# Kernel tuning notes

Hardware: AMD Instinct MI355X
Metric: run time of the kernel (lower is better)

The kernel has to match this reference:

```python
import jax, jax.numpy as jnp
import numpy as np

N_NODES = 50000
N_EDGES = 800000
IN_DIM, HID_DIM, OUT_DIM = 128, 128, 256


def _gcn_conv(x, W, b, src, dst, num_nodes):
    # PyG GCNConv: h = D^{-1/2} (A + I) D^{-1/2} X W + b (self-loops already in src/dst)
    h = x @ W  # (N, F_out)
    ones = jnp.ones(src.shape[0], dtype=h.dtype)
    deg = jax.ops.segment_sum(ones, dst, num_segments=num_nodes)
    dinv = jnp.where(deg > 0, jax.lax.rsqrt(deg), 0.0)
    norm = dinv[src] * dinv[dst]  # (E,)
    msg = h[src] * norm[:, None]  # (E, F_out) gather
    out = jax.ops.segment_sum(msg, dst, num_segments=num_nodes)  # scatter-add
    return out + b


def setup_inputs() -> dict:
    key = jax.random.key(0)
    ks = jax.random.split(key, 6)
    x = jax.random.normal(ks[0], (N_NODES, IN_DIM), dtype=jnp.float32)
    edge_index = jax.random.randint(ks[1], (2, N_EDGES), 0, N_NODES, dtype=jnp.int64)
    W1 = jax.random.normal(ks[2], (IN_DIM, HID_DIM), dtype=jnp.float32) / np.sqrt(IN_DIM)
    b1 = jnp.zeros((HID_DIM,), jnp.float32)
    W2 = jax.random.normal(ks[3], (HID_DIM, OUT_DIM), dtype=jnp.float32) / np.sqrt(HID_DIM)
    b2 = jnp.zeros((OUT_DIM,), jnp.float32)
    Wa = jax.random.normal(ks[4], (OUT_DIM, 1), dtype=jnp.float32) / np.sqrt(OUT_DIM)
    ba = jnp.zeros((1,), jnp.float32)
    return {"x": x, "edge_index": edge_index, "W1": W1, "b1": b1, "W2": W2, "b2": b2, "Wa": Wa, "ba": ba}


def reference(x, edge_index, W1, b1, W2, b2, Wa, ba):
    n = x.shape[0]
    loops = jnp.arange(n, dtype=edge_index.dtype)
    src = jnp.concatenate([edge_index[0], loops])
    dst = jnp.concatenate([edge_index[1], loops])
    h = jax.nn.relu(_gcn_conv(x, W1, b1, src, dst, n))
    # dropout is a no-op in eval mode
    node_embeddings = jax.nn.relu(_gcn_conv(h, W2, b2, src, dst, n))
    logits = node_embeddings @ Wa + ba  # (N, 1)
    attn = jax.nn.softmax(logits, axis=0)  # softmax over nodes
    graph_embedding = jnp.sum(node_embeddings * attn, axis=0, keepdims=True)  # (1, OUT_DIM)
    return (node_embeddings, graph_embedding)
```

## Files before the change

### kernel.cpp

```cpp
#include <hip/hip_runtime.h>
#include <hip/hip_fp16.h>
#include <math.h>

typedef __attribute__((ext_vector_type(8))) short bf16x8;
typedef __attribute__((ext_vector_type(4))) float f32x4;

static __device__ __forceinline__ unsigned short f2bf(float x) {
    unsigned u = __float_as_uint(x);
    unsigned r = (u + 0x7FFF + ((u >> 16) & 1)) >> 16;
    return (unsigned short)r;
}
static __device__ __forceinline__ float bf2f(unsigned short h) {
    return __uint_as_float(((unsigned)h) << 16);
}
static __device__ __forceinline__ void addh8(float* a, uint4 v) {
    float2 f;
    f = __half22float2(*(const __half2*)&v.x); a[0] += f.x; a[1] += f.y;
    f = __half22float2(*(const __half2*)&v.y); a[2] += f.x; a[3] += f.y;
    f = __half22float2(*(const __half2*)&v.z); a[4] += f.x; a[5] += f.y;
    f = __half22float2(*(const __half2*)&v.w); a[6] += f.x; a[7] += f.y;
}


__global__ __launch_bounds__(256) void count_deg_kernel(const int* __restrict__ dst, int E,
                                                        int* __restrict__ deg,
                                                        int* __restrict__ epos) {
    int e = blockIdx.x * 256 + threadIdx.x;
    if (e < E) epos[e] = atomicAdd(&deg[dst[e]], 1);
}

__global__ __launch_bounds__(256) void scan_partial_kernel(const int* __restrict__ deg, int n,
                                                           int* __restrict__ partials) {
    int idx = blockIdx.x * 1024 + threadIdx.x * 4;
    int4 v = make_int4(0, 0, 0, 0);
    if (idx + 3 < n) v = *(const int4*)(deg + idx);
    else {
        if (idx < n) v.x = deg[idx];
        if (idx + 1 < n) v.y = deg[idx + 1];
        if (idx + 2 < n) v.z = deg[idx + 2];
    }
    int s = v.x + v.y + v.z + v.w;
    for (int off = 1; off < 64; off <<= 1) s += __shfl_xor(s, off);
    __shared__ int sm[4];
    int wave = threadIdx.x >> 6;
    if ((threadIdx.x & 63) == 0) sm[wave] = s;
    __syncthreads();
    if (threadIdx.x == 0) partials[blockIdx.x] = sm[0] + sm[1] + sm[2] + sm[3];
}

__global__ __launch_bounds__(256) void scan_final_kernel(const int* __restrict__ deg, int n,
                                                         const int* __restrict__ partials, int nbk,
                                                         int* __restrict__ rowptr) {
    int idx = blockIdx.x * 1024 + threadIdx.x * 4;
    int4 v = make_int4(0, 0, 0, 0);
    if (idx + 3 < n) v = *(const int4*)(deg + idx);
    else {
        if (idx < n) v.x = deg[idx];
        if (idx + 1 < n) v.y = deg[idx + 1];
        if (idx + 2 < n) v.z = deg[idx + 2];
    }
    int tsum = v.x + v.y + v.z + v.w;
    int lane = threadIdx.x & 63, wave = threadIdx.x >> 6;
    int s = tsum;
    for (int off = 1; off < 64; off <<= 1) {
        int u = __shfl_up(s, off);
        if (lane >= off) s += u;
    }
    __shared__ int wsum[4];
    __shared__ int bb;
    if (lane == 63) wsum[wave] = s;
    if (threadIdx.x < 64) {
        int pv = (threadIdx.x < nbk) ? partials[threadIdx.x] : 0;
        int ps = pv;
        for (int off = 1; off < 64; off <<= 1) {
            int u = __shfl_up(ps, off);
            if (threadIdx.x >= off) ps += u;
        }
        if (threadIdx.x == blockIdx.x) bb = ps - pv;
        if (blockIdx.x == 0 && threadIdx.x == 63) rowptr[n] = ps;
    }
    __syncthreads();
    int base = bb;
    for (int w = 0; w < wave; ++w) base += wsum[w];
    int e0 = base + s - tsum;
    int4 o;
    o.x = e0; o.y = e0 + v.x; o.z = o.y + v.y; o.w = o.z + v.z;
    if (idx + 3 < n) *(int4*)(rowptr + idx) = o;
    else {
        if (idx < n) rowptr[idx] = o.x;
        if (idx + 1 < n) rowptr[idx + 1] = o.y;
        if (idx + 2 < n) rowptr[idx + 2] = o.z;
    }
}


__global__ __launch_bounds__(256) void prep_kernel(
    const int* __restrict__ src, const int* __restrict__ dst, const int* __restrict__ epos, int E,
    const int* __restrict__ rowptr, int* __restrict__ csrsrc, int scatterBlocks,
    const float* __restrict__ x, float* __restrict__ dinv,
    __half2* __restrict__ xs16, int n, int prescaleBlocks,
    const float* __restrict__ W1, const float* __restrict__ W2,
    unsigned short* __restrict__ w1h, unsigned short* __restrict__ w1l,
    unsigned short* __restrict__ w2h, unsigned short* __restrict__ w2l) {
    int b = blockIdx.x;
    if (b < scatterBlocks) {
        int e = b * 256 + threadIdx.x;
        if (e < E) csrsrc[rowptr[dst[e]] + epos[e]] = src[e];
    } else if (b < scatterBlocks + prescaleBlocks) {
        int node = (b - scatterBlocks) * 4 + (threadIdx.x >> 6);
        int lane = threadIdx.x & 63;
        if (node >= n) return;
        float di = rsqrtf((float)(rowptr[node + 1] - rowptr[node] + 1));
        if (lane == 0) dinv[node] = di;
        float2 v = *(const float2*)(x + (size_t)node * 128 + (lane << 1));
        xs16[(size_t)node * 64 + lane] = __floats2half2_rn(di * v.x, di * v.y);
    } else {
        int i = (b - scatterBlocks - prescaleBlocks) * 256 + threadIdx.x;
        if (i < 128 * 128) {
            int nn = i >> 7, k = i & 127;
            float v = W1[k * 128 + nn];
            unsigned short h = f2bf(v);
            w1h[nn * 128 + k] = h;
            w1l[nn * 128 + k] = f2bf(v - bf2f(h));
        } else if (i < 128 * 128 + 256 * 128) {
            int j = i - 128 * 128;
            int nn = j >> 7, k = j & 127;
            float v = W2[k * 256 + nn];
            unsigned short h = f2bf(v);
            w2h[nn * 128 + k] = h;
            w2l[nn * 128 + k] = f2bf(v - bf2f(h));
        }
    }
}


template <int NCOLS, bool SCALE_DINV, bool DO_LOGITS, bool OUT_F16>
__global__ __launch_bounds__(512, 2) void fused_gemm(
    const unsigned short* __restrict__ X16,
    const int* __restrict__ rowptr, const int* __restrict__ csrsrc,
    const float* __restrict__ dinv,
    const unsigned short* __restrict__ Bth, const unsigned short* __restrict__ Btl,
    const float* __restrict__ bias, void* __restrict__ Cout, int M,
    const float* __restrict__ Wa, float* __restrict__ logits) {
    constexpr int CT = NCOLS / 64;
    __shared__ unsigned short AsH[128 * 128];
    __shared__ unsigned short AsL[128 * 128];

    const int t = threadIdx.x;
    const int row0 = blockIdx.x * 128;

    {
        const int nl = t >> 2;
        const int sub = t & 3;
        const int row = row0 + nl;
        float acc[32];
#pragma unroll
        for (int i = 0; i < 32; ++i) acc[i] = 0.f;
        float di = 0.f;
        if (row < M) {
            const uint4* __restrict__ Xv = (const uint4*)X16;
            size_t sb = (size_t)row * 16 + sub * 4;
            uint4 v0 = Xv[sb], v1 = Xv[sb + 1], v2 = Xv[sb + 2], v3 = Xv[sb + 3];
            addh8(acc, v0); addh8(acc + 8, v1); addh8(acc + 16, v2); addh8(acc + 24, v3);
            int e1 = rowptr[row + 1];
            int e = rowptr[row];
            for (; e + 2 <= e1; e += 2) {
                int s0 = csrsrc[e], s1 = csrsrc[e + 1];
                size_t b0 = (size_t)s0 * 16 + sub * 4;
                size_t b1 = (size_t)s1 * 16 + sub * 4;
                uint4 a0 = Xv[b0], a1 = Xv[b0 + 1], a2 = Xv[b0 + 2], a3 = Xv[b0 + 3];
                uint4 c0 = Xv[b1], c1 = Xv[b1 + 1], c2 = Xv[b1 + 2], c3 = Xv[b1 + 3];
                addh8(acc, a0); addh8(acc + 8, a1); addh8(acc + 16, a2); addh8(acc + 24, a3);
                addh8(acc, c0); addh8(acc + 8, c1); addh8(acc + 16, c2); addh8(acc + 24, c3);
            }
            if (e < e1) {
                size_t b0 = (size_t)csrsrc[e] * 16 + sub * 4;
                uint4 a0 = Xv[b0], a1 = Xv[b0 + 1], a2 = Xv[b0 + 2], a3 = Xv[b0 + 3];
                addh8(acc, a0); addh8(acc + 8, a1); addh8(acc + 16, a2); addh8(acc + 24, a3);
            }
            di = dinv[row];
        }
#pragma unroll
        for (int j = 0; j < 4; ++j) {
            int ga = sub * 4 + j;
            int off = nl * 128 + (ga >> 3) * 64 + (((ga & 7) ^ (nl & 7)) << 3);
            unsigned short h[8], l[8];
#pragma unroll
            for (int q = 0; q < 8; ++q) {
                float f = di * acc[j * 8 + q];
                h[q] = f2bf(f);
                l[q] = f2bf(f - bf2f(h[q]));
            }
            uint4 hv, lv;
            hv.x = (unsigned)h[0] | ((unsigned)h[1] << 16);
            hv.y = (unsigned)h[2] | ((unsigned)h[3] << 16);
            hv.z = (unsigned)h[4] | ((unsigned)h[5] << 16);
            hv.w = (unsigned)h[6] | ((unsigned)h[7] << 16);
            lv.x = (unsigned)l[0] | ((unsigned)l[1] << 16);
            lv.y = (unsigned)l[2] | ((unsigned)l[3] << 16);
            lv.z = (unsigned)l[4] | ((unsigned)l[5] << 16);
            lv.w = (unsigned)l[6] | ((unsigned)l[7] << 16);
            *(uint4*)(AsH + off) = hv;
            *(uint4*)(AsL + off) = lv;
        }
    }
    __syncthreads();

    const int lane = t & 63;
    const int wave = t >> 6;
    const int wrow = wave >> 2;
    const int wcol = wave & 3;
    const int lq = lane >> 4;
    const int lm = lane & 15;

    f32x4 acc2[4][CT] = {};
    float lacc[4][4] = {};

#pragma unroll
    for (int kc = 0; kc < 2; ++kc)
#pragma unroll
        for (int ks = 0; ks < 2; ++ks) {
            const int gbase = ks * 4 + lq;
            bf16x8 ah[4], al[4], bh[CT], bl[CT];
#pragma unroll
            for (int rt = 0; rt < 4; ++rt) {
                int ra = wrow * 64 + rt * 16 + lm;
                int off = ra * 128 + kc * 64 + ((gbase ^ (ra & 7)) << 3);
                ah[rt] = *(const bf16x8*)(AsH + off);
                al[rt] = *(const bf16x8*)(AsL + off);
            }
#pragma unroll
            for (int ct = 0; ct < CT; ++ct) {
                int col = wcol * (16 * CT) + ct * 16 + lm;
                size_t bo = (size_t)col * 128 + kc * 64 + gbase * 8;
                bh[ct] = *(const bf16x8*)(Bth + bo);
                bl[ct] = *(const bf16x8*)(Btl + bo);
            }
#pragma unroll
            for (int rt = 0; rt < 4; ++rt)
#pragma unroll
                for (int ct = 0; ct < CT; ++ct) {
                    acc2[rt][ct] = __builtin_amdgcn_mfma_f32_16x16x32_bf16(ah[rt], bh[ct], acc2[rt][ct], 0, 0, 0);
                    acc2[rt][ct] = __builtin_amdgcn_mfma_f32_16x16x32_bf16(al[rt], bh[ct], acc2[rt][ct], 0, 0, 0);
                    acc2[rt][ct] = __builtin_amdgcn_mfma_f32_16x16x32_bf16(ah[rt], bl[ct], acc2[rt][ct], 0, 0, 0);
                }
        }

#pragma unroll
    for (int ct = 0; ct < CT; ++ct) {
        int col = wcol * (16 * CT) + ct * 16 + lm;
        float bc = bias[col];
        float wac = DO_LOGITS ? Wa[col] : 0.f;
#pragma unroll
        for (int rt = 0; rt < 4; ++rt) {
            int rowb = row0 + wrow * 64 + rt * 16 + lq * 4;
#pragma unroll
            for (int reg = 0; reg < 4; ++reg) {
                int gr = rowb + reg;
                if (gr < M) {
                    float o = fmaxf(acc2[rt][ct][reg] + bc, 0.f);
                    if (SCALE_DINV) o *= dinv[gr];
                    if (OUT_F16) ((__half*)Cout)[(size_t)gr * NCOLS + col] = __float2half(o);
                    else ((float*)Cout)[(size_t)gr * NCOLS + col] = o;
                    if (DO_LOGITS) lacc[rt][reg] += o * wac;
                }
            }
        }
    }

    if (DO_LOGITS) {
#pragma unroll
        for (int rt = 0; rt < 4; ++rt)
#pragma unroll
            for (int reg = 0; reg < 4; ++reg) {
                float s = lacc[rt][reg];
                s += __shfl_xor(s, 1);
                s += __shfl_xor(s, 2);
                s += __shfl_xor(s, 4);
                s += __shfl_xor(s, 8);
                int gr = row0 + wrow * 64 + rt * 16 + lq * 4 + reg;
                if (lm == 0 && gr < M) atomicAdd(&logits[gr], s);
            }
    }
}


__global__ __launch_bounds__(256) void maxsum_kernel(const float* __restrict__ logits, int n,
                                                     float2* __restrict__ part,
                                                     float* __restrict__ outTail) {
    if (blockIdx.x == 0) outTail[threadIdx.x] = 0.f;
    float m = -INFINITY, s = 0.f;
    for (int i = blockIdx.x * 256 + threadIdx.x; i < n; i += gridDim.x * 256) {
        float v = logits[i];
        if (v > m) { s = s * expf(m - v) + 1.f; m = v; }
        else s += expf(v - m);
    }
    __shared__ float sm[256], ss[256];
    sm[threadIdx.x] = m; ss[threadIdx.x] = s;
    __syncthreads();
    for (int off = 128; off > 0; off >>= 1) {
        if (threadIdx.x < off) {
            float m1 = sm[threadIdx.x], s1 = ss[threadIdx.x];
            float m2 = sm[threadIdx.x + off], s2 = ss[threadIdx.x + off];
            float M = fmaxf(m1, m2);
            sm[threadIdx.x] = M;
            ss[threadIdx.x] = s1 * expf(m1 - M) + s2 * expf(m2 - M);
        }
        __syncthreads();
    }
    if (threadIdx.x == 0) part[blockIdx.x] = make_float2(sm[0], ss[0]);
}

static __device__ __forceinline__ float2 merge_part(const float2* __restrict__ part, int t,
                                                    float* red2) {
    if (t < 64) {
        float2 p = part[t];
        float m = p.x, s = p.y;
        for (int off = 32; off > 0; off >>= 1) {
            float m2 = __shfl_xor(m, off);
            float s2 = __shfl_xor(s, off);
            float M = fmaxf(m, m2);
            s = s * expf(m - M) + s2 * expf(m2 - M);
            m = M;
        }
        if (t == 0) { red2[0] = m; red2[1] = s; }
    }
    __syncthreads();
    return make_float2(red2[0], red2[1]);
}

__global__ __launch_bounds__(256) void weighted_sum_kernel(const float* __restrict__ emb,
                                                           const float* __restrict__ logits,
                                                           const float2* __restrict__ part,
                                                           float* __restrict__ gpart, int n) {
    __shared__ float red2[2];
    float g = merge_part(part, threadIdx.x, red2).x;
    int wave = threadIdx.x >> 6;
    int lane = threadIdx.x & 63;
    int stride = gridDim.x * 4;
    float4 acc = make_float4(0.f, 0.f, 0.f, 0.f);
#pragma unroll 2
    for (int r = blockIdx.x * 4 + wave; r < n; r += stride) {
        float w = expf(logits[r] - g);
        float4 v = *(const float4*)(emb + (size_t)r * 256 + (lane << 2));
        acc.x += w * v.x; acc.y += w * v.y; acc.z += w * v.z; acc.w += w * v.w;
    }
    __shared__ float4 sm[256];
    sm[threadIdx.x] = acc;
    __syncthreads();
    if (wave == 0) {
        float4 a = sm[lane], b = sm[64 + lane], c = sm[128 + lane], d = sm[192 + lane];
        float4 s;
        s.x = (a.x + b.x) + (c.x + d.x);
        s.y = (a.y + b.y) + (c.y + d.y);
        s.z = (a.z + b.z) + (c.z + d.z);
        s.w = (a.w + b.w) + (c.w + d.w);
        *(float4*)(gpart + (size_t)blockIdx.x * 256 + (lane << 2)) = s;
    }
}

__global__ __launch_bounds__(256) void reduce_gpart_kernel(const float* __restrict__ gpart,
                                                           const float2* __restrict__ part,
                                                           float* __restrict__ outTail, int nb) {
    __shared__ float red2[2];
    float gsum = merge_part(part, threadIdx.x, red2).y;
    int rows = nb / gridDim.x;
    int r0 = blockIdx.x * rows;
    float s = 0.f;
    for (int r = r0; r < r0 + rows; ++r) s += gpart[(size_t)r * 256 + threadIdx.x];
    atomicAdd(&outTail[threadIdx.x], s / gsum);
}


extern "C" void kernel_launch(void* const* d_in, const int* in_sizes, int n_in,
                              void* d_out, int out_size, void* d_ws, size_t ws_size,
                              hipStream_t stream) {
    const float* x  = (const float*)d_in[0];
    const int* ei   = (const int*)d_in[1];
    const float* W1 = (const float*)d_in[2];
    const float* b1 = (const float*)d_in[3];
    const float* W2 = (const float*)d_in[4];
    const float* b2 = (const float*)d_in[5];
    const float* Wa = (const float*)d_in[6];
    float* out = (float*)d_out;

    const int n = in_sizes[0] / 128;
    const int E = in_sizes[1] / 2;
    const int* srcA = ei;
    const int* dstA = ei + E;
    const int nb = (n + 1023) / 1024;
    const int WS_BLOCKS = 1024;

    unsigned short* xs16 = (unsigned short*)d_ws;
    unsigned short* h16  = xs16 + (size_t)n * 128;
    unsigned short* w1h  = h16 + (size_t)n * 128;
    unsigned short* w1l  = w1h + 128 * 128;
    unsigned short* w2h  = w1l + 128 * 128;
    unsigned short* w2l  = w2h + 256 * 128;
    float* dinv   = (float*)(w2l + 256 * 128);
    float* logits = dinv + n;
    int* deg      = (int*)(logits + n);
    int* rowptr   = deg + n;
    int* partials = rowptr + n + 1;
    float2* part  = (float2*)(partials + 64);
    float* gpart  = (float*)(part + 64);
    int* epos     = (int*)(gpart + WS_BLOCKS * 256);
    int* csrsrc   = epos + E;

    hipMemsetAsync(logits, 0, sizeof(float) * (size_t)(2 * n), stream);

    count_deg_kernel<<<(E + 255) / 256, 256, 0, stream>>>(dstA, E, deg, epos);
    scan_partial_kernel<<<nb, 256, 0, stream>>>(deg, n, partials);
    scan_final_kernel<<<nb, 256, 0, stream>>>(deg, n, partials, nb, rowptr);

    int scatterBlocks = (E + 255) / 256;
    int prescaleBlocks = (n + 3) / 4;
    int wconvBlocks = (128 * 128 + 256 * 128 + 255) / 256;
    prep_kernel<<<scatterBlocks + prescaleBlocks + wconvBlocks, 256, 0, stream>>>(
        srcA, dstA, epos, E, rowptr, csrsrc, scatterBlocks,
        x, dinv, (__half2*)xs16, n, prescaleBlocks,
        W1, W2, w1h, w1l, w2h, w2l);

    int gemmRows = (n + 127) / 128;

    fused_gemm<128, true, false, true><<<gemmRows, 512, 0, stream>>>(
        xs16, rowptr, csrsrc, dinv, w1h, w1l, b1, h16, n, nullptr, nullptr);
    fused_gemm<256, false, true, false><<<gemmRows, 512, 0, stream>>>(
        h16, rowptr, csrsrc, dinv, w2h, w2l, b2, out, n, Wa, logits);

    maxsum_kernel<<<64, 256, 0, stream>>>(logits, n, part, out + (size_t)n * 256);
    weighted_sum_kernel<<<WS_BLOCKS, 256, 0, stream>>>(out, logits, part, gpart, n);
    reduce_gpart_kernel<<<32, 256, 0, stream>>>(gpart, part, out + (size_t)n * 256, WS_BLOCKS);
}
```

Measured before the change: 296.8 us.

## Halve fused GEMM row tile to 64 and raise occupancy with 8 threads per node

The fused aggregate+GEMM kernel now processes 64 rows per block instead of 128, with 8 threads per node each gathering 16 features and the edge loop unrolled by 4. The wave layout changes so each wave owns one 16-row strip and half the output columns, which shrinks the accumulator register footprint and LDS use. Launch bounds go from 2 to 8 blocks per CU to raise occupancy and hide gather latency. The cost is less reuse of B fragments per wave, more B loads from global/L2 per MFMA, and more blocks overall.

```diff
diff --git a/kernel.cpp b/kernel.cpp
--- a/kernel.cpp
+++ b/kernel.cpp
@@ -135,54 +135,60 @@
 
 
 template <int NCOLS, bool SCALE_DINV, bool DO_LOGITS, bool OUT_F16>
-__global__ __launch_bounds__(512, 2) void fused_gemm(
+__global__ __launch_bounds__(512, 8) void fused_gemm(
     const unsigned short* __restrict__ X16,
     const int* __restrict__ rowptr, const int* __restrict__ csrsrc,
     const float* __restrict__ dinv,
     const unsigned short* __restrict__ Bth, const unsigned short* __restrict__ Btl,
     const float* __restrict__ bias, void* __restrict__ Cout, int M,
     const float* __restrict__ Wa, float* __restrict__ logits) {
-    constexpr int CT = NCOLS / 64;
-    __shared__ unsigned short AsH[128 * 128];
-    __shared__ unsigned short AsL[128 * 128];
+    constexpr int CT = NCOLS / 32;
+    __shared__ unsigned short AsH[64 * 128];
+    __shared__ unsigned short AsL[64 * 128];
 
     const int t = threadIdx.x;
-    const int row0 = blockIdx.x * 128;
+    const int row0 = blockIdx.x * 64;
 
     {
-        const int nl = t >> 2;
-        const int sub = t & 3;
+        const int nl = t >> 3;
+        const int sub = t & 7;
         const int row = row0 + nl;
-        float acc[32];
-#pragma unroll
-        for (int i = 0; i < 32; ++i) acc[i] = 0.f;
+        float acc[16];
+#pragma unroll
+        for (int i = 0; i < 16; ++i) acc[i] = 0.f;
         float di = 0.f;
         if (row < M) {
             const uint4* __restrict__ Xv = (const uint4*)X16;
-            size_t sb = (size_t)row * 16 + sub * 4;
-            uint4 v0 = Xv[sb], v1 = Xv[sb + 1], v2 = Xv[sb + 2], v3 = Xv[sb + 3];
-            addh8(acc, v0); addh8(acc + 8, v1); addh8(acc + 16, v2); addh8(acc + 24, v3);
+            size_t sb = (size_t)row * 16 + sub * 2;
+            uint4 v0 = Xv[sb], v1 = Xv[sb + 1];
+            addh8(acc, v0); addh8(acc + 8, v1);
             int e1 = rowptr[row + 1];
             int e = rowptr[row];
-            for (; e + 2 <= e1; e += 2) {
-                int s0 = csrsrc[e], s1 = csrsrc[e + 1];
-                size_t b0 = (size_t)s0 * 16 + sub * 4;
-                size_t b1 = (size_t)s1 * 16 + sub * 4;
-                uint4 a0 = Xv[b0], a1 = Xv[b0 + 1], a2 = Xv[b0 + 2], a3 = Xv[b0 + 3];
-                uint4 c0 = Xv[b1], c1 = Xv[b1 + 1], c2 = Xv[b1 + 2], c3 = Xv[b1 + 3];
-                addh8(acc, a0); addh8(acc + 8, a1); addh8(acc + 16, a2); addh8(acc + 24, a3);
-                addh8(acc, c0); addh8(acc + 8, c1); addh8(acc + 16, c2); addh8(acc + 24, c3);
+            for (; e + 4 <= e1; e += 4) {
+                int s0 = csrsrc[e], s1 = csrsrc[e + 1], s2 = csrsrc[e + 2], s3 = csrsrc[e + 3];
+                size_t b0 = (size_t)s0 * 16 + sub * 2;
+                size_t b1 = (size_t)s1 * 16 + sub * 2;
+                size_t b2 = (size_t)s2 * 16 + sub * 2;
+                size_t b3 = (size_t)s3 * 16 + sub * 2;
+                uint4 a0 = Xv[b0], a1 = Xv[b0 + 1];
+                uint4 c0 = Xv[b1], c1 = Xv[b1 + 1];
+                uint4 d0 = Xv[b2], d1 = Xv[b2 + 1];
+                uint4 f0 = Xv[b3], f1 = Xv[b3 + 1];
+                addh8(acc, a0); addh8(acc + 8, a1);
+                addh8(acc, c0); addh8(acc + 8, c1);
+                addh8(acc, d0); addh8(acc + 8, d1);
+                addh8(acc, f0); addh8(acc + 8, f1);
             }
-            if (e < e1) {
-                size_t b0 = (size_t)csrsrc[e] * 16 + sub * 4;
-                uint4 a0 = Xv[b0], a1 = Xv[b0 + 1], a2 = Xv[b0 + 2], a3 = Xv[b0 + 3];
-                addh8(acc, a0); addh8(acc + 8, a1); addh8(acc + 16, a2); addh8(acc + 24, a3);
+            for (; e < e1; ++e) {
+                size_t b0 = (size_t)csrsrc[e] * 16 + sub * 2;
+                uint4 a0 = Xv[b0], a1 = Xv[b0 + 1];
+                addh8(acc, a0); addh8(acc + 8, a1);
             }
             di = dinv[row];
         }
 #pragma unroll
-        for (int j = 0; j < 4; ++j) {
-            int ga = sub * 4 + j;
+        for (int j = 0; j < 2; ++j) {
+            int ga = sub * 2 + j;
             int off = nl * 128 + (ga >> 3) * 64 + (((ga & 7) ^ (nl & 7)) << 3);
             unsigned short h[8], l[8];
 #pragma unroll
@@ -208,79 +214,65 @@
 
     const int lane = t & 63;
     const int wave = t >> 6;
-    const int wrow = wave >> 2;
-    const int wcol = wave & 3;
+    const int wrow = wave & 3;
+    const int wcol = wave >> 2;
     const int lq = lane >> 4;
     const int lm = lane & 15;
 
-    f32x4 acc2[4][CT] = {};
-    float lacc[4][4] = {};
+    f32x4 acc2[CT] = {};
+    float lacc[4] = {0.f, 0.f, 0.f, 0.f};
 
 #pragma unroll
     for (int kc = 0; kc < 2; ++kc)
 #pragma unroll
         for (int ks = 0; ks < 2; ++ks) {
             const int gbase = ks * 4 + lq;
-            bf16x8 ah[4], al[4], bh[CT], bl[CT];
-#pragma unroll
-            for (int rt = 0; rt < 4; ++rt) {
-                int ra = wrow * 64 + rt * 16 + lm;
-                int off = ra * 128 + kc * 64 + ((gbase ^ (ra & 7)) << 3);
-                ah[rt] = *(const bf16x8*)(AsH + off);
-                al[rt] = *(const bf16x8*)(AsL + off);
+            const int ra = wrow * 16 + lm;
+            const int aoff = ra * 128 + kc * 64 + ((gbase ^ (ra & 7)) << 3);
+            bf16x8 ah = *(const bf16x8*)(AsH + aoff);
+            bf16x8 al = *(const bf16x8*)(AsL + aoff);
+#pragma unroll
+            for (int ct = 0; ct < CT; ++ct) {
+                int col = wcol * (NCOLS / 2) + ct * 16 + lm;
+                size_t bo = (size_t)col * 128 + kc * 64 + gbase * 8;
+                bf16x8 bh = *(const bf16x8*)(Bth + bo);
+                bf16x8 bl = *(const bf16x8*)(Btl + bo);
+                acc2[ct] = __builtin_amdgcn_mfma_f32_16x16x32_bf16(ah, bh, acc2[ct], 0, 0, 0);
+                acc2[ct] = __builtin_amdgcn_mfma_f32_16x16x32_bf16(al, bh, acc2[ct], 0, 0, 0);
+                acc2[ct] = __builtin_amdgcn_mfma_f32_16x16x32_bf16(ah, bl, acc2[ct], 0, 0, 0);
             }
-#pragma unroll
-            for (int ct = 0; ct < CT; ++ct) {
-                int col = wcol * (16 * CT) + ct * 16 + lm;
-                size_t bo = (size_t)col * 128 + kc * 64 + gbase * 8;
-                bh[ct] = *(const bf16x8*)(Bth + bo);
-                bl[ct] = *(const bf16x8*)(Btl + bo);
-            }
-#pragma unroll
-            for (int rt = 0; rt < 4; ++rt)
-#pragma unroll
-                for (int ct = 0; ct < CT; ++ct) {
-                    acc2[rt][ct] = __builtin_amdgcn_mfma_f32_16x16x32_bf16(ah[rt], bh[ct], acc2[rt][ct], 0, 0, 0);
-                    acc2[rt][ct] = __builtin_amdgcn_mfma_f32_16x16x32_bf16(al[rt], bh[ct], acc2[rt][ct], 0, 0, 0);
-                    acc2[rt][ct] = __builtin_amdgcn_mfma_f32_16x16x32_bf16(ah[rt], bl[ct], acc2[rt][ct], 0, 0, 0);
-                }
         }
 
 #pragma unroll
     for (int ct = 0; ct < CT; ++ct) {
-        int col = wcol * (16 * CT) + ct * 16 + lm;
+        int col = wcol * (NCOLS / 2) + ct * 16 + lm;
         float bc = bias[col];
         float wac = DO_LOGITS ? Wa[col] : 0.f;
-#pragma unroll
-        for (int rt = 0; rt < 4; ++rt) {
-            int rowb = row0 + wrow * 64 + rt * 16 + lq * 4;
-#pragma unroll
-            for (int reg = 0; reg < 4; ++reg) {
-                int gr = rowb + reg;
-                if (gr < M) {
-                    float o = fmaxf(acc2[rt][ct][reg] + bc, 0.f);
-                    if (SCALE_DINV) o *= dinv[gr];
-                    if (OUT_F16) ((__half*)Cout)[(size_t)gr * NCOLS + col] = __float2half(o);
-                    else ((float*)Cout)[(size_t)gr * NCOLS + col] = o;
-                    if (DO_LOGITS) lacc[rt][reg] += o * wac;
-                }
+        int rowb = row0 + wrow * 16 + lq * 4;
+#pragma unroll
+        for (int reg = 0; reg < 4; ++reg) {
+            int gr = rowb + reg;
+            if (gr < M) {
+                float o = fmaxf(acc2[ct][reg] + bc, 0.f);
+                if (SCALE_DINV) o *= dinv[gr];
+                if (OUT_F16) ((__half*)Cout)[(size_t)gr * NCOLS + col] = __float2half(o);
+                else ((float*)Cout)[(size_t)gr * NCOLS + col] = o;
+                if (DO_LOGITS) lacc[reg] += o * wac;
             }
         }
     }
 
     if (DO_LOGITS) {
 #pragma unroll
-        for (int rt = 0; rt < 4; ++rt)
-#pragma unroll
-            for (int reg = 0; reg < 4; ++reg) {
-                float s = lacc[rt][reg];
-                s += __shfl_xor(s, 1);
-                s += __shfl_xor(s, 2);
-                s += __shfl_xor(s, 4);
-                s += __shfl_xor(s, 8);
-                int gr = row0 + wrow * 64 + rt * 16 + lq * 4 + reg;
-                if (lm == 0 && gr < M) atomicAdd(&logits[gr], s);
-            }
+        for (int reg = 0; reg < 4; ++reg) {
+            float s = lacc[reg];
+            s += __shfl_xor(s, 1);
+            s += __shfl_xor(s, 2);
+            s += __shfl_xor(s, 4);
+            s += __shfl_xor(s, 8);
+            int gr = row0 + wrow * 16 + lq * 4 + reg;
+            if (lm == 0 && gr < M) atomicAdd(&logits[gr], s);
+        }
     }
 }
 
@@ -421,7 +413,7 @@
         x, dinv, (__half2*)xs16, n, prescaleBlocks,
         W1, W2, w1h, w1l, w2h, w2l);
 
-    int gemmRows = (n + 127) / 128;
+    int gemmRows = (n + 63) / 64;
 
     fused_gemm<128, true, false, true><<<gemmRows, 512, 0, stream>>>(
         xs16, rowptr, csrsrc, dinv, w1h, w1l, b1, h16, n, nullptr, nullptr);
```

After: 366.0 us. 23.3% more time.
